# Kernel optimization log

Hardware: AMD Instinct MI355X
Metric: run time of the kernel (lower is better)

The kernel has to match this reference:

```python
import jax, jax.numpy as jnp
import numpy as np

PAD = 0  # pad_token_id sentinel used for word_starts and labels_arcs masking


def setup_inputs() -> dict:
    B, S, H, L = 16, 256, 768, 37
    key = jax.random.key(0)
    k1, k2, k3, k4, k5 = jax.random.split(key, 5)
    hidden = jax.random.normal(k1, (B, S, H), dtype=jnp.float32)
    # strictly-increasing subword start indices (1,3,5,...), zero-padded to S
    n_starts = S // 2
    row = jnp.concatenate([
        1 + 2 * jnp.arange(n_starts, dtype=jnp.int32),
        jnp.zeros(S - n_starts, dtype=jnp.int32),
    ])
    word_starts = jnp.tile(row[None, :], (B, 1))
    n_words = n_starts - 1  # spans are between consecutive starts
    la = jax.random.randint(k2, (B, S), 1, 2 * S, dtype=jnp.int32)
    labels_arcs = jnp.where(jnp.arange(S)[None, :] < n_words, la, PAD)
    labels_rels = jax.random.randint(k3, (B, S), 0, L, dtype=jnp.int32)
    W_arc = jax.random.normal(k4, (H + 1, H), dtype=jnp.float32) * 0.02
    W_rel = jax.random.normal(k5, (L, H + 1, H + 1), dtype=jnp.float32) * 0.02
    return dict(hidden=hidden, W_arc=W_arc, W_rel=W_rel,
                word_starts=word_starts, labels_arcs=labels_arcs,
                labels_rels=labels_rels)


def _merge_subword_tokens(hidden, word_starts):
    """Fused segment-mean: word j = mean(hidden[start_j:start_{j+1}])."""
    B, S, H = hidden.shape
    csum = jnp.concatenate(
        [jnp.zeros((B, 1, H), hidden.dtype), jnp.cumsum(hidden, axis=1)], axis=1)
    n_valid = jnp.sum(word_starts != PAD, axis=1)  # [B]
    start = word_starts  # [B,S]
    end = jnp.concatenate(
        [word_starts[:, 1:], jnp.zeros((B, 1), word_starts.dtype)], axis=1)
    valid = (jnp.arange(S)[None, :] + 1) < n_valid[:, None]  # word j needs start j+1
    s0 = jnp.take_along_axis(csum, start[..., None].astype(jnp.int32), axis=1)
    s1 = jnp.take_along_axis(csum, end[..., None].astype(jnp.int32), axis=1)
    length = jnp.clip(end - start, 1, None).astype(hidden.dtype)[..., None]
    return jnp.where(valid[..., None], (s1 - s0) / length, 0.0)  # [B,S,H]


def _with_ones(x):
    return jnp.concatenate([x, jnp.ones_like(x[..., :1])], axis=-1)


def reference(hidden, W_arc, W_rel, word_starts, labels_arcs, labels_rels):
    deps = _merge_subword_tokens(hidden, word_starts)            # [B,S,H]
    heads = jnp.concatenate([hidden, deps], axis=1)              # [B,2S,H]
    xa = _with_ones(deps)                                        # [B,S,H+1]
    arc_preds = jnp.einsum('bxi,ij,byj->bxy', xa, W_arc, heads)  # [B,S,2S]
    yr = _with_ones(heads)                                       # [B,2S,H+1]
    rel_preds = jnp.einsum('bxi,oij,byj->bxyo', xa, W_rel, yr)   # [B,S,2S,L]

    B, S, Y, L = rel_preds.shape
    mask = (labels_arcs != PAD).astype(hidden.dtype)             # [B,S]
    n = jnp.sum(mask)
    arc_lp = jax.nn.log_softmax(arc_preds, axis=-1)
    safe_arcs = jnp.clip(labels_arcs, 0, Y - 1)
    arc_ll = jnp.take_along_axis(arc_lp, safe_arcs[..., None], axis=-1)[..., 0]
    arc_loss = -jnp.sum(arc_ll * mask) / n

    idx = jnp.broadcast_to(safe_arcs[:, :, None, None], (B, S, 1, L))
    rel_sel = jnp.take_along_axis(rel_preds, idx, axis=2)[:, :, 0, :]  # [B,S,L]
    rel_lp = jax.nn.log_softmax(rel_sel, axis=-1)
    rel_ll = jnp.take_along_axis(rel_lp, labels_rels[..., None], axis=-1)[..., 0]
    rel_loss = -jnp.sum(rel_ll * mask) / n

    loss = arc_loss + rel_loss
    return loss, rel_preds, arc_preds
```

## Files before the change

### kernel.cpp

```cpp
#include <hip/hip_runtime.h>
#include <cmath>
#include <cstdint>


#define NB 16
#define SS 256
#define HH 768
#define LLn 37
#define YY 512

static const long long REL_ELEMS = (long long)NB * SS * YY * LLn;

typedef __bf16 bf16_t;
typedef __bf16 bf16x8 __attribute__((ext_vector_type(8)));
typedef float f32x4 __attribute__((ext_vector_type(4)));

__device__ __forceinline__ void async_copy16(const void* g, void* l) {
  __builtin_amdgcn_global_load_lds((__attribute__((address_space(1))) void*)(g),
                                   (__attribute__((address_space(3))) void*)(l),
                                   16, 0, 0);
}


__global__ void hid_rows(const float* __restrict__ hidden, bf16_t* __restrict__ yrb) {
  const long long r = blockIdx.x;
  const int b = (int)(r >> 8), y = (int)(r & 255);
  const float* src = hidden + r * HH;
  bf16_t* dst = yrb + ((long long)b * YY + y) * HH;
  for (int h = threadIdx.x; h < HH; h += 256) dst[h] = (bf16_t)src[h];
}

__global__ void build_deps2(const float* __restrict__ hidden,
                            const int* __restrict__ word_starts,
                            bf16_t* __restrict__ yrb) {
  const int x = blockIdx.x, b = blockIdx.y, t = threadIdx.x;
  const int ws0 = word_starts[b * SS + x];
  const int ws1 = (x + 1 < SS) ? word_starts[b * SS + x + 1] : 0;
  const bool valid = (x + 1 < SS) && (ws1 != 0);
  const int start = min(max(ws0, 0), SS);
  const int end = min(max(ws1, 0), SS);
  const int len = max(end - start, 1);
  const float inv = 1.0f / (float)len;
  const float* hb = hidden + (long long)b * SS * HH;
  bf16_t* yr = yrb + ((long long)b * YY + SS + x) * HH;
  for (int h = t; h < HH; h += 256) {
    float s = 0.f;
    if (valid) for (int tt = start; tt < end; ++tt) s += hb[(long long)tt * HH + h];
    yr[h] = (bf16_t)(valid ? s * inv : 0.f);
  }
}

__global__ void conv_warc(const float* __restrict__ W, bf16_t* __restrict__ Wab) {
  __shared__ float tbuf[32][33];
  const int i0 = blockIdx.x * 32, j0 = blockIdx.y * 32;
  const int tx = threadIdx.x, ty = threadIdx.y;
  for (int rr = 0; rr < 32; rr += 8)
    tbuf[ty + rr][tx] = W[(long long)(i0 + ty + rr) * HH + j0 + tx];
  __syncthreads();
  for (int rr = 0; rr < 32; rr += 8)
    Wab[(long long)(j0 + ty + rr) * HH + i0 + tx] = (bf16_t)tbuf[tx][ty + rr];
}

__global__ void conv_wrel(const float* __restrict__ W, bf16_t* __restrict__ Wb, int o0) {
  __shared__ float tbuf[32][33];
  const int o = o0 + blockIdx.z;
  const int i0 = blockIdx.x * 32, j0 = blockIdx.y * 32;
  const int tx = threadIdx.x, ty = threadIdx.y;
  const float* Wo = W + (long long)o * (HH + 1) * (HH + 1);
  for (int rr = 0; rr < 32; rr += 8)
    tbuf[ty + rr][tx] = Wo[(long long)(i0 + ty + rr) * (HH + 1) + j0 + tx];
  __syncthreads();
  bf16_t* Wbo = Wb + (long long)blockIdx.z * HH * HH;
  for (int rr = 0; rr < 32; rr += 8)
    Wbo[(long long)(j0 + ty + rr) * HH + i0 + tx] = (bf16_t)tbuf[tx][ty + rr];
}

__global__ void build_misc(const float* __restrict__ W_rel, const float* __restrict__ W_arc,
                           float* __restrict__ WbiasJ, bf16_t* __restrict__ Wb768,
                           float* __restrict__ bias768b, float* __restrict__ biasArc,
                           float* __restrict__ lossacc) {
  const int blk = blockIdx.x, t = threadIdx.x;
  if (blk < LLn) {
    const int o = blk;
    const float* Wo = W_rel + (long long)o * (HH + 1) * (HH + 1);
    for (int j = t; j < HH; j += 256)
      WbiasJ[(long long)o * HH + j] = Wo[(long long)HH * (HH + 1) + j];
    for (int i = t; i < HH; i += 256)
      Wb768[(long long)o * HH + i] = (bf16_t)Wo[(long long)i * (HH + 1) + HH];
    if (t == 0) bias768b[o] = Wo[(long long)HH * (HH + 1) + HH];
  } else if (blk == LLn) {
    for (int j = t; j < HH; j += 256) biasArc[j] = W_arc[(long long)HH * HH + j];
    if (t == 0) { lossacc[0] = 0.f; lossacc[1] = 0.f; }
  } else {
    for (int i = t; i < (128 - LLn) * HH; i += 256) Wb768[(long long)LLn * HH + i] = (bf16_t)0.f;
    if (t + LLn < 128) bias768b[t + LLn] = 0.f;
  }
}


template<int RT, int MODE>
__global__ __launch_bounds__(256)
void gemm_bt(const bf16_t* __restrict__ A, long long sAz, int lda, int aview,
             const bf16_t* __restrict__ B, long long sBz, int ldb,
             int K,
             float* __restrict__ Cf, bf16_t* __restrict__ Cb,
             long long sCz, int ldc,
             const float* __restrict__ cbias, int sbias,
             int OC, int o0, const float* __restrict__ bias_xo) {
  constexpr int SM0 = RT * 8192 + 8192;
  constexpr int SMEM = SM0 > 16896 ? SM0 : 16896;
  __shared__ __align__(16) char smem_raw[SMEM];
  bf16_t* As = (bf16_t*)smem_raw;
  bf16_t* Bs = (bf16_t*)(smem_raw + RT * 8192);
  const int tid = threadIdx.x;
  const int w = tid >> 6;
  const int lane = tid & 63;
  const int z = blockIdx.z;
  const long long row0 = (long long)blockIdx.y * (RT * 128);
  const long long col0 = (long long)blockIdx.x * 128;
  const bf16_t* Ab;
  if (aview) {
    const long long bb = row0 >> 8;
    Ab = A + (bb * 512 + 256 + (row0 & 255)) * (long long)lda;
  } else {
    Ab = A + z * sAz + row0 * lda;
  }
  const bf16_t* Bb = B + z * sBz + col0 * ldb;

  const int r_in = lane >> 2;
  const int kofs = (lane & 3) * 8;
  const bf16_t* gA[2 * RT];
  bf16_t* lA[2 * RT];
  #pragma unroll
  for (int c = 0; c < 2 * RT; c++) {
    gA[c] = Ab + (long long)(w * (32 * RT) + c * 16 + r_in) * lda + kofs;
    lA[c] = &As[(w * (32 * RT) + c * 16) * 32];
  }
  const bf16_t* gB0 = Bb + (long long)(w * 32 + r_in) * ldb + kofs;
  const bf16_t* gB1 = gB0 + 16ll * ldb;
  bf16_t* lB0 = &Bs[(w * 32) * 32];
  bf16_t* lB1 = &Bs[(w * 32 + 16) * 32];

  f32x4 acc[4 * RT][4];
  #pragma unroll
  for (int i = 0; i < 4 * RT; i++)
    #pragma unroll
    for (int j = 0; j < 4; j++)
      #pragma unroll
      for (int e = 0; e < 4; e++) acc[i][j][e] = 0.f;

  const int wm = (w >> 1) * (64 * RT), wn = (w & 1) * 64;
  const int fr = lane & 15;
  const int fq = lane >> 4;
  const int aoff = fq * 8;

  for (int k0 = 0; k0 < K; k0 += 32) {
    #pragma unroll
    for (int c = 0; c < 2 * RT; c++) async_copy16(gA[c] + k0, lA[c]);
    async_copy16(gB0 + k0, lB0);
    async_copy16(gB1 + k0, lB1);
    __syncthreads();
    bf16x8 bfr[4];
    #pragma unroll
    for (int t = 0; t < 4; t++) bfr[t] = *(const bf16x8*)&Bs[(wn + t * 16 + fr) * 32 + aoff];
    #pragma unroll
    for (int tm = 0; tm < 4 * RT; tm++) {
      const bf16x8 af = *(const bf16x8*)&As[(wm + tm * 16 + fr) * 32 + aoff];
      #pragma unroll
      for (int tn = 0; tn < 4; tn++)
        acc[tm][tn] = __builtin_amdgcn_mfma_f32_16x16x32_bf16(af, bfr[tn], acc[tm][tn], 0, 0, 0);
    }
    __syncthreads();
  }

  if (MODE == 2) {
    float* ebuf = (float*)smem_raw;
    const int c = tid & 127;
    const int rgrp = tid >> 7;
    const int n = (int)col0 + c;
    const int x = n / OC;
    const int o = o0 + (n - x * OC);
    const float bias = bias_xo[(((long long)z << 8) + x) * 128 + o];
    float* outp = Cf + z * sCz + (long long)x * (YY * LLn) + o;
    #pragma unroll
    for (int ch = 0; ch < 4 * RT; ch++) {
      #pragma unroll
      for (int tn = 0; tn < 4; tn++)
        #pragma unroll
        for (int e = 0; e < 4; e++)
          ebuf[((w >> 1) * 16 + fq * 4 + e) * 132 + wn + tn * 16 + fr] = acc[ch][tn][e];
      __syncthreads();
      const long long ybase = row0 + (long long)rgrp * (64 * RT) + ch * 16;
      #pragma unroll
      for (int r = 0; r < 16; r++)
        outp[(ybase + r) * LLn] = ebuf[(rgrp * 16 + r) * 132 + c] + bias;
      __syncthreads();
    }
  } else {
    const int er = fq * 4;
    #pragma unroll
    for (int tn = 0; tn < 4; tn++) {
      const long long col = col0 + wn + tn * 16 + fr;
      const float bv = cbias ? cbias[(long long)z * sbias + col] : 0.f;
      #pragma unroll
      for (int tm = 0; tm < 4 * RT; tm++) {
        const int rl = wm + tm * 16 + er;
        if (MODE == 0) {
          bf16_t* dst = Cb + z * sCz + col;
          #pragma unroll
          for (int r = 0; r < 4; r++)
            dst[(row0 + rl + r) * (long long)ldc] = (bf16_t)(acc[tm][tn][r] + bv);
        } else {
          float* dst = Cf + z * sCz + col;
          #pragma unroll
          for (int r = 0; r < 4; r++)
            dst[(row0 + rl + r) * (long long)ldc] = acc[tm][tn][r] + bv;
        }
      }
    }
  }
}


__device__ __forceinline__ float wave_max(float v) {
  #pragma unroll
  for (int off = 32; off > 0; off >>= 1) v = fmaxf(v, __shfl_xor(v, off));
  return v;
}
__device__ __forceinline__ float wave_sum(float v) {
  #pragma unroll
  for (int off = 32; off > 0; off >>= 1) v += __shfl_xor(v, off);
  return v;
}

__global__ void loss_kernel(const float* __restrict__ arc, const float* __restrict__ rel,
                            const int* __restrict__ la, const int* __restrict__ lr,
                            float* __restrict__ acc) {
  const int r = blockIdx.x;
  const int lane = threadIdx.x;
  const int lab = la[r];
  const float* ar = arc + (long long)r * YY;
  float v[8]; float m = -INFINITY;
  #pragma unroll
  for (int i = 0; i < 8; i++) { v[i] = ar[lane + 64 * i]; m = fmaxf(m, v[i]); }
  m = wave_max(m);
  float s = 0.f;
  #pragma unroll
  for (int i = 0; i < 8; i++) s += expf(v[i] - m);
  s = wave_sum(s);
  const float lse_a = m + logf(s);
  const int safe = lab < 0 ? 0 : (lab > YY - 1 ? YY - 1 : lab);
  const float* rr = rel + ((long long)r * YY + safe) * LLn;
  const float rv = (lane < LLn) ? rr[lane] : -INFINITY;
  const float m2 = wave_max(rv);
  const float s2 = wave_sum((lane < LLn) ? expf(rv - m2) : 0.f);
  const float lse_r = m2 + logf(s2);
  if (lane == 0 && lab != 0) {
    const float ll = (ar[safe] - lse_a) + (rr[lr[r]] - lse_r);
    atomicAdd(&acc[0], ll);
    atomicAdd(&acc[1], 1.f);
  }
}

__global__ void finalize(const float* __restrict__ acc, float* __restrict__ out) {
  out[0] = -acc[0] / acc[1];
}


extern "C" void kernel_launch(void* const* d_in, const int* in_sizes, int n_in,
                              void* d_out, int out_size, void* d_ws, size_t ws_size,
                              hipStream_t stream) {
  (void)in_sizes; (void)n_in; (void)out_size;
  const float* hidden      = (const float*)d_in[0];
  const float* W_arc       = (const float*)d_in[1];
  const float* W_rel       = (const float*)d_in[2];
  const int* word_starts   = (const int*)d_in[3];
  const int* labels_arcs   = (const int*)d_in[4];
  const int* labels_rels   = (const int*)d_in[5];

  float* out = (float*)d_out;
  float* rel_out = out + 1;
  float* arc_out = rel_out + REL_ELEMS;

  char* ws = (char*)d_ws;
  float* lossacc  = (float*)ws;
  bf16_t* yrb     = (bf16_t*)(ws + 256);
  bf16_t* Wab     = yrb + (size_t)NB * YY * HH;
  bf16_t* A1      = Wab + (size_t)HH * HH;
  bf16_t* Wb768   = A1 + (size_t)NB * SS * HH;
  float*  biasArc = (float*)(Wb768 + (size_t)128 * HH);
  float*  bias768b= biasArc + HH;
  float*  d_bias2 = bias768b + 128;
  float*  WbiasJ  = d_bias2 + (size_t)NB * SS * 128;
  bf16_t* Wbc     = (bf16_t*)(WbiasJ + (size_t)LLn * HH);

  const size_t fixedB = 256 +
      2 * ((size_t)NB * YY * HH + (size_t)HH * HH + (size_t)NB * SS * HH +
           (size_t)128 * HH) +
      4 * ((size_t)HH + 128 + (size_t)NB * SS * 128 + (size_t)LLn * HH);
  const size_t perOC = 2 * ((size_t)HH * HH + (size_t)NB * SS * HH);
  int OC = 1;
  if (ws_size > fixedB + perOC) {
    const size_t m = (ws_size - fixedB) / perOC;
    OC = (m > (size_t)LLn) ? LLn : (int)m;
  }
  bf16_t* M_p = Wbc + (size_t)OC * HH * HH;

  hid_rows<<<NB * SS, 256, 0, stream>>>(hidden, yrb);
  build_deps2<<<dim3(SS, NB), 256, 0, stream>>>(hidden, word_starts, yrb);
  conv_warc<<<dim3(24, 24), dim3(32, 8), 0, stream>>>(W_arc, Wab);
  build_misc<<<39, 256, 0, stream>>>(W_rel, W_arc, WbiasJ, Wb768, bias768b, biasArc, lossacc);

  gemm_bt<1, 0><<<dim3(6, 32, 1), 256, 0, stream>>>(
      yrb, 0, HH, 1, Wab, 0, HH, HH,
      nullptr, A1, 0, HH, biasArc, 0, 0, 0, nullptr);
  gemm_bt<1, 1><<<dim3(4, 2, NB), 256, 0, stream>>>(
      A1, (long long)SS * HH, HH, 0,
      yrb, (long long)YY * HH, HH, HH,
      arc_out, nullptr, (long long)SS * YY, YY, nullptr, 0, 0, 0, nullptr);
  gemm_bt<1, 1><<<dim3(1, 32, 1), 256, 0, stream>>>(
      yrb, 0, HH, 1, Wb768, 0, HH, HH,
      d_bias2, nullptr, 0, 128, bias768b, 0, 0, 0, nullptr);

  for (int o0 = 0; o0 < LLn; o0 += OC) {
    const int oc = (LLn - o0 < OC) ? (LLn - o0) : OC;
    conv_wrel<<<dim3(24, 24, oc), dim3(32, 8), 0, stream>>>(W_rel, Wbc, o0);
    gemm_bt<2, 0><<<dim3(6, 16, oc), 256, 0, stream>>>(
        yrb, 0, HH, 1,
        Wbc, (long long)HH * HH, HH, HH,
        nullptr, M_p, HH, oc * HH, WbiasJ + (long long)o0 * HH, HH, 0, 0, nullptr);
    gemm_bt<2, 2><<<dim3(2 * oc, 2, NB), 256, 0, stream>>>(
        yrb, (long long)YY * HH, HH, 0,
        M_p, (long long)SS * oc * HH, HH, HH,
        rel_out, nullptr, (long long)SS * YY * LLn, 0, nullptr, 0,
        oc, o0, d_bias2);
  }

  loss_kernel<<<NB * SS, 64, 0, stream>>>(arc_out, rel_out, labels_arcs, labels_rels, lossacc);
  finalize<<<1, 1, 0, stream>>>(lossacc, out);
}
```

Measured before the change: 1.199 ms.

## Double-buffer GEMM LDS tiles, shrink row tile, vectorize conversion, add bias2 dot kernel

The GEMM kernel now double-buffers its LDS tiles, issuing async global-to-LDS loads for the next K slice while MFMAs run on the current one, which removes one barrier per iteration. It also drops the RT=2 row tiling, so the big rel GEMMs launch twice as many 128-row blocks. The hid_rows conversion now reads float4 and writes four bf16 values per thread. The padded 128-wide d_bias2 GEMM is replaced by a per-row dot-product kernel over only the 37 real labels, which no longer needs zeroed pad rows. The costs are more LDS per block, which may lower occupancy, and less register reuse from the smaller tiles.

```diff
diff --git a/kernel.cpp b/kernel.cpp
--- a/kernel.cpp
+++ b/kernel.cpp
@@ -21,13 +21,27 @@
                                    16, 0, 0);
 }
 
+__device__ __forceinline__ float wave_max(float v) {
+  #pragma unroll
+  for (int off = 32; off > 0; off >>= 1) v = fmaxf(v, __shfl_xor(v, off));
+  return v;
+}
+__device__ __forceinline__ float wave_sum(float v) {
+  #pragma unroll
+  for (int off = 32; off > 0; off >>= 1) v += __shfl_xor(v, off);
+  return v;
+}
+
 
 __global__ void hid_rows(const float* __restrict__ hidden, bf16_t* __restrict__ yrb) {
   const long long r = blockIdx.x;
   const int b = (int)(r >> 8), y = (int)(r & 255);
-  const float* src = hidden + r * HH;
+  const float4* src = (const float4*)(hidden + r * HH);
   bf16_t* dst = yrb + ((long long)b * YY + y) * HH;
-  for (int h = threadIdx.x; h < HH; h += 256) dst[h] = (bf16_t)src[h];
+  const int t = threadIdx.x;
+  const float4 v = src[t];
+  bf16_t o4[4] = {(bf16_t)v.x, (bf16_t)v.y, (bf16_t)v.z, (bf16_t)v.w};
+  *(ushort4*)(dst + t * 4) = *(ushort4*)o4;
 }
 
 __global__ void build_deps2(const float* __restrict__ hidden,
@@ -88,17 +102,35 @@
     for (int i = t; i < HH; i += 256)
       Wb768[(long long)o * HH + i] = (bf16_t)Wo[(long long)i * (HH + 1) + HH];
     if (t == 0) bias768b[o] = Wo[(long long)HH * (HH + 1) + HH];
-  } else if (blk == LLn) {
+  } else {
     for (int j = t; j < HH; j += 256) biasArc[j] = W_arc[(long long)HH * HH + j];
     if (t == 0) { lossacc[0] = 0.f; lossacc[1] = 0.f; }
-  } else {
-    for (int i = t; i < (128 - LLn) * HH; i += 256) Wb768[(long long)LLn * HH + i] = (bf16_t)0.f;
-    if (t + LLn < 128) bias768b[t + LLn] = 0.f;
-  }
-}
-
-
-template<int RT, int MODE>
+  }
+}
+
+__global__ void bias2_kernel(const bf16_t* __restrict__ yrb,
+                             const bf16_t* __restrict__ Wb768,
+                             const float* __restrict__ bias768b,
+                             float* __restrict__ d_bias2) {
+  const int r = blockIdx.x;
+  const int b = r >> 8, x = r & 255;
+  const bf16_t* dep = yrb + ((long long)b * YY + SS + x) * HH;
+  const int w = threadIdx.x >> 6, lane = threadIdx.x & 63;
+  __shared__ float drow[HH];
+  for (int h = threadIdx.x; h < HH; h += 256) drow[h] = (float)dep[h];
+  __syncthreads();
+  for (int o = w; o < LLn; o += 4) {
+    const bf16_t* wrow = Wb768 + (long long)o * HH;
+    float s = 0.f;
+    #pragma unroll
+    for (int i = 0; i < HH / 64; i++) s += drow[lane + 64 * i] * (float)wrow[lane + 64 * i];
+    s = wave_sum(s);
+    if (lane == 0) d_bias2[(long long)r * 128 + o] = s + bias768b[o];
+  }
+}
+
+
+template<int MODE>
 __global__ __launch_bounds__(256)
 void gemm_bt(const bf16_t* __restrict__ A, long long sAz, int lda, int aview,
              const bf16_t* __restrict__ B, long long sBz, int ldb,
@@ -107,16 +139,13 @@
              long long sCz, int ldc,
              const float* __restrict__ cbias, int sbias,
              int OC, int o0, const float* __restrict__ bias_xo) {
-  constexpr int SM0 = RT * 8192 + 8192;
-  constexpr int SMEM = SM0 > 16896 ? SM0 : 16896;
-  __shared__ __align__(16) char smem_raw[SMEM];
-  bf16_t* As = (bf16_t*)smem_raw;
-  bf16_t* Bs = (bf16_t*)(smem_raw + RT * 8192);
+  __shared__ __align__(16) char smem_raw[32768];
+  bf16_t* const lds = (bf16_t*)smem_raw;
   const int tid = threadIdx.x;
   const int w = tid >> 6;
   const int lane = tid & 63;
   const int z = blockIdx.z;
-  const long long row0 = (long long)blockIdx.y * (RT * 128);
+  const long long row0 = (long long)blockIdx.y * 128;
   const long long col0 = (long long)blockIdx.x * 128;
   const bf16_t* Ab;
   if (aview) {
@@ -129,51 +158,71 @@
 
   const int r_in = lane >> 2;
   const int kofs = (lane & 3) * 8;
-  const bf16_t* gA[2 * RT];
-  bf16_t* lA[2 * RT];
-  #pragma unroll
-  for (int c = 0; c < 2 * RT; c++) {
-    gA[c] = Ab + (long long)(w * (32 * RT) + c * 16 + r_in) * lda + kofs;
-    lA[c] = &As[(w * (32 * RT) + c * 16) * 32];
-  }
+  const bf16_t* gA0 = Ab + (long long)(w * 32 + r_in) * lda + kofs;
+  const bf16_t* gA1 = gA0 + 16ll * lda;
   const bf16_t* gB0 = Bb + (long long)(w * 32 + r_in) * ldb + kofs;
   const bf16_t* gB1 = gB0 + 16ll * ldb;
-  bf16_t* lB0 = &Bs[(w * 32) * 32];
-  bf16_t* lB1 = &Bs[(w * 32 + 16) * 32];
-
-  f32x4 acc[4 * RT][4];
-  #pragma unroll
-  for (int i = 0; i < 4 * RT; i++)
+  const int lA0 = (w * 32) * 32;
+  const int lA1 = (w * 32 + 16) * 32;
+  const int lB0 = 4096 + (w * 32) * 32;
+  const int lB1 = 4096 + (w * 32 + 16) * 32;
+
+  f32x4 acc[4][4];
+  #pragma unroll
+  for (int i = 0; i < 4; i++)
     #pragma unroll
     for (int j = 0; j < 4; j++)
       #pragma unroll
       for (int e = 0; e < 4; e++) acc[i][j][e] = 0.f;
 
-  const int wm = (w >> 1) * (64 * RT), wn = (w & 1) * 64;
+  const int wm = (w >> 1) * 64, wn = (w & 1) * 64;
   const int fr = lane & 15;
   const int fq = lane >> 4;
   const int aoff = fq * 8;
 
-  for (int k0 = 0; k0 < K; k0 += 32) {
-    #pragma unroll
-    for (int c = 0; c < 2 * RT; c++) async_copy16(gA[c] + k0, lA[c]);
-    async_copy16(gB0 + k0, lB0);
-    async_copy16(gB1 + k0, lB1);
+  async_copy16(gA0, lds + lA0);
+  async_copy16(gA1, lds + lA1);
+  async_copy16(gB0, lds + lB0);
+  async_copy16(gB1, lds + lB1);
+  __syncthreads();
+
+  int cur = 0;
+  for (int k0 = 32; k0 < K; k0 += 32) {
+    bf16_t* nb = lds + (cur ^ 1) * 8192;
+    async_copy16(gA0 + k0, nb + lA0);
+    async_copy16(gA1 + k0, nb + lA1);
+    async_copy16(gB0 + k0, nb + lB0);
+    async_copy16(gB1 + k0, nb + lB1);
+    const bf16_t* cb = lds + cur * 8192;
+    bf16x8 af[4], bfr[4];
+    #pragma unroll
+    for (int t = 0; t < 4; t++) af[t]  = *(const bf16x8*)&cb[(wm + t * 16 + fr) * 32 + aoff];
+    #pragma unroll
+    for (int t = 0; t < 4; t++) bfr[t] = *(const bf16x8*)&cb[4096 + (wn + t * 16 + fr) * 32 + aoff];
+    #pragma unroll
+    for (int tm = 0; tm < 4; tm++)
+      #pragma unroll
+      for (int tn = 0; tn < 4; tn++)
+        acc[tm][tn] = __builtin_amdgcn_mfma_f32_16x16x32_bf16(af[tm], bfr[tn], acc[tm][tn], 0, 0, 0);
     __syncthreads();
-    bf16x8 bfr[4];
-    #pragma unroll
-    for (int t = 0; t < 4; t++) bfr[t] = *(const bf16x8*)&Bs[(wn + t * 16 + fr) * 32 + aoff];
-    #pragma unroll
-    for (int tm = 0; tm < 4 * RT; tm++) {
-      const bf16x8 af = *(const bf16x8*)&As[(wm + tm * 16 + fr) * 32 + aoff];
+    cur ^= 1;
+  }
+  {
+    const bf16_t* cb = lds + cur * 8192;
+    bf16x8 af[4], bfr[4];
+    #pragma unroll
+    for (int t = 0; t < 4; t++) af[t]  = *(const bf16x8*)&cb[(wm + t * 16 + fr) * 32 + aoff];
+    #pragma unroll
+    for (int t = 0; t < 4; t++) bfr[t] = *(const bf16x8*)&cb[4096 + (wn + t * 16 + fr) * 32 + aoff];
+    #pragma unroll
+    for (int tm = 0; tm < 4; tm++)
       #pragma unroll
       for (int tn = 0; tn < 4; tn++)
-        acc[tm][tn] = __builtin_amdgcn_mfma_f32_16x16x32_bf16(af, bfr[tn], acc[tm][tn], 0, 0, 0);
-    }
+        acc[tm][tn] = __builtin_amdgcn_mfma_f32_16x16x32_bf16(af[tm], bfr[tn], acc[tm][tn], 0, 0, 0);
+  }
+
+  if (MODE == 2) {
     __syncthreads();
-  }
-
-  if (MODE == 2) {
     float* ebuf = (float*)smem_raw;
     const int c = tid & 127;
     const int rgrp = tid >> 7;
@@ -183,14 +232,14 @@
     const float bias = bias_xo[(((long long)z << 8) + x) * 128 + o];
     float* outp = Cf + z * sCz + (long long)x * (YY * LLn) + o;
     #pragma unroll
-    for (int ch = 0; ch < 4 * RT; ch++) {
+    for (int ch = 0; ch < 4; ch++) {
       #pragma unroll
       for (int tn = 0; tn < 4; tn++)
         #pragma unroll
         for (int e = 0; e < 4; e++)
           ebuf[((w >> 1) * 16 + fq * 4 + e) * 132 + wn + tn * 16 + fr] = acc[ch][tn][e];
       __syncthreads();
-      const long long ybase = row0 + (long long)rgrp * (64 * RT) + ch * 16;
+      const long long ybase = row0 + (long long)rgrp * 64 + ch * 16;
       #pragma unroll
       for (int r = 0; r < 16; r++)
         outp[(ybase + r) * LLn] = ebuf[(rgrp * 16 + r) * 132 + c] + bias;
@@ -203,7 +252,7 @@
       const long long col = col0 + wn + tn * 16 + fr;
       const float bv = cbias ? cbias[(long long)z * sbias + col] : 0.f;
       #pragma unroll
-      for (int tm = 0; tm < 4 * RT; tm++) {
+      for (int tm = 0; tm < 4; tm++) {
         const int rl = wm + tm * 16 + er;
         if (MODE == 0) {
           bf16_t* dst = Cb + z * sCz + col;
@@ -222,17 +271,6 @@
 }
 
 
-__device__ __forceinline__ float wave_max(float v) {
-  #pragma unroll
-  for (int off = 32; off > 0; off >>= 1) v = fmaxf(v, __shfl_xor(v, off));
-  return v;
-}
-__device__ __forceinline__ float wave_sum(float v) {
-  #pragma unroll
-  for (int off = 32; off > 0; off >>= 1) v += __shfl_xor(v, off);
-  return v;
-}
-
 __global__ void loss_kernel(const float* __restrict__ arc, const float* __restrict__ rel,
                             const int* __restrict__ la, const int* __restrict__ lr,
                             float* __restrict__ acc) {
@@ -306,30 +344,28 @@
   }
   bf16_t* M_p = Wbc + (size_t)OC * HH * HH;
 
-  hid_rows<<<NB * SS, 256, 0, stream>>>(hidden, yrb);
+  hid_rows<<<NB * SS, 192, 0, stream>>>(hidden, yrb);
   build_deps2<<<dim3(SS, NB), 256, 0, stream>>>(hidden, word_starts, yrb);
   conv_warc<<<dim3(24, 24), dim3(32, 8), 0, stream>>>(W_arc, Wab);
-  build_misc<<<39, 256, 0, stream>>>(W_rel, W_arc, WbiasJ, Wb768, bias768b, biasArc, lossacc);
-
-  gemm_bt<1, 0><<<dim3(6, 32, 1), 256, 0, stream>>>(
+  build_misc<<<LLn + 1, 256, 0, stream>>>(W_rel, W_arc, WbiasJ, Wb768, bias768b, biasArc, lossacc);
+  bias2_kernel<<<NB * SS, 256, 0, stream>>>(yrb, Wb768, bias768b, d_bias2);
+
+  gemm_bt<0><<<dim3(6, 32, 1), 256, 0, stream>>>(
       yrb, 0, HH, 1, Wab, 0, HH, HH,
       nullptr, A1, 0, HH, biasArc, 0, 0, 0, nullptr);
-  gemm_bt<1, 1><<<dim3(4, 2, NB), 256, 0, stream>>>(
+  gemm_bt<1><<<dim3(4, 2, NB), 256, 0, stream>>>(
       A1, (long long)SS * HH, HH, 0,
       yrb, (long long)YY * HH, HH, HH,
       arc_out, nullptr, (long long)SS * YY, YY, nullptr, 0, 0, 0, nullptr);
-  gemm_bt<1, 1><<<dim3(1, 32, 1), 256, 0, stream>>>(
-      yrb, 0, HH, 1, Wb768, 0, HH, HH,
-      d_bias2, nullptr, 0, 128, bias768b, 0, 0, 0, nullptr);
 
   for (int o0 = 0; o0 < LLn; o0 += OC) {
     const int oc = (LLn - o0 < OC) ? (LLn - o0) : OC;
     conv_wrel<<<dim3(24, 24, oc), dim3(32, 8), 0, stream>>>(W_rel, Wbc, o0);
-    gemm_bt<2, 0><<<dim3(6, 16, oc), 256, 0, stream>>>(
+    gemm_bt<0><<<dim3(6, 32, oc), 256, 0, stream>>>(
         yrb, 0, HH, 1,
         Wbc, (long long)HH * HH, HH, HH,
         nullptr, M_p, HH, oc * HH, WbiasJ + (long long)o0 * HH, HH, 0, 0, nullptr);
-    gemm_bt<2, 2><<<dim3(2 * oc, 2, NB), 256, 0, stream>>>(
+    gemm_bt<2><<<dim3(2 * oc, 4, NB), 256, 0, stream>>>(
         yrb, (long long)YY * HH, HH, 0,
         M_p, (long long)SS * oc * HH, HH, HH,
         rel_out, nullptr, (long long)SS * YY * LLn, 0, nullptr, 0,
```

After: 998.9 us. 1.2x faster.
